# Kernel optimization log

Hardware: AMD Instinct MI355X
Metric: run time of the kernel (lower is better)

Reference implementation:

```python
import jax, jax.numpy as jnp
import numpy as np

N = 50000      # nodes
E = 600000     # edges
G = 256        # graphs in batch
H = 128        # hidden channels
EPS = 1e-5     # batchnorm eps


def gcn_conv(x, W, b, src, dst, n):
    """PyG GCNConv: h = x W; symmetric-normalized aggregation with self-loops."""
    h = x @ W  # [n, H]
    ones = jnp.ones(src.shape[0], dtype=x.dtype)
    deg = jax.ops.segment_sum(ones, dst, num_segments=n) + 1.0  # in-degree + self-loop
    dis = jax.lax.rsqrt(deg)  # deg^{-1/2}
    msg = (dis[src] * dis[dst])[:, None] * h[src]  # [E, H] gathered messages
    agg = jax.ops.segment_sum(msg, dst, num_segments=n)
    return agg + (dis * dis)[:, None] * h + b  # self-loop contribution + bias


def batch_norm(x, gamma, beta):
    m = x.mean(axis=0)
    v = x.var(axis=0)  # biased variance, as torch BN uses for normalization
    return gamma * (x - m) * jax.lax.rsqrt(v + EPS) + beta


def setup_inputs() -> dict:
    key = jax.random.key(0)
    ks = jax.random.split(key, 12)
    x = jax.random.normal(ks[0], (N, H), dtype=jnp.float32)
    edge_index = jax.random.randint(ks[1], (2, E), 0, N, dtype=jnp.int32)
    batch = jnp.sort(jax.random.randint(ks[2], (N,), 0, G, dtype=jnp.int32))
    s = 1.0 / np.sqrt(H)
    W1 = jax.random.uniform(ks[3], (H, H), jnp.float32, -s, s)
    b1 = jnp.zeros((H,), jnp.float32)
    g1 = jnp.ones((H,), jnp.float32)
    be1 = jnp.zeros((H,), jnp.float32)
    W2 = jax.random.uniform(ks[4], (H, H), jnp.float32, -s, s)
    b2 = jnp.zeros((H,), jnp.float32)
    g2 = jnp.ones((H,), jnp.float32)
    be2 = jnp.zeros((H,), jnp.float32)
    W3 = jax.random.uniform(ks[5], (H, H), jnp.float32, -s, s)
    b3 = jnp.zeros((H,), jnp.float32)
    Wl = jax.random.uniform(ks[6], (H, 1), jnp.float32, -s, s)
    bl = jnp.zeros((1,), jnp.float32)
    return {"x": x, "edge_index": edge_index, "batch": batch,
            "W1": W1, "b1": b1, "g1": g1, "be1": be1,
            "W2": W2, "b2": b2, "g2": g2, "be2": be2,
            "W3": W3, "b3": b3, "Wl": Wl, "bl": bl}


def reference(x, edge_index, batch, W1, b1, g1, be1, W2, b2, g2, be2, W3, b3, Wl, bl):
    src, dst = edge_index[0], edge_index[1]
    h = gcn_conv(x, W1, b1, src, dst, N)
    h = jax.nn.relu(batch_norm(h, g1, be1))  # dropout is identity in eval mode
    h = gcn_conv(h, W2, b2, src, dst, N)
    h = jax.nn.relu(batch_norm(h, g2, be2))
    h = jax.nn.relu(gcn_conv(h, W3, b3, src, dst, N))
    sums = jax.ops.segment_sum(h, batch, num_segments=G)           # [G, H]
    cnt = jax.ops.segment_sum(jnp.ones((N,), h.dtype), batch, num_segments=G)
    pooled = sums / jnp.maximum(cnt, 1.0)[:, None]                  # global mean pool
    return pooled @ Wl + bl                                         # [G, 1]
```

## Files before the change

kernel.cpp:

```cpp
#include <hip/hip_runtime.h>
#include <cstdint>

#define NN 50000
#define NE 600000
#define NGR 256
#define HD 128
#define HD2 64
#define BN_EPS 1e-5f

static __device__ __forceinline__ unsigned f2bf(float f) {
  unsigned u = __float_as_uint(f);
  return (u + 0x7FFFu + ((u >> 16) & 1u)) >> 16;
}
static __device__ __forceinline__ float bf_lo(unsigned v) {
  return __uint_as_float(v << 16);
}
static __device__ __forceinline__ float bf_hi(unsigned v) {
  return __uint_as_float(v & 0xFFFF0000u);
}

__global__ void k_zero(float4* __restrict__ p, int n4) {
  int i = blockIdx.x * blockDim.x + threadIdx.x;
  if (i < n4) p[i] = make_float4(0.f, 0.f, 0.f, 0.f);
}

__global__ void k_count(const int* __restrict__ dst, int* __restrict__ cnt) {
  int i = blockIdx.x * blockDim.x + threadIdx.x;
  if (i < NE) atomicAdd(&cnt[dst[i]], 1);
}

__global__ __launch_bounds__(1024) void k_scan1(const int* __restrict__ cnt,
                                                int* __restrict__ rowptr,
                                                int* __restrict__ aux,
                                                float* __restrict__ dis) {
  __shared__ int sd[1024];
  int tid = threadIdx.x;
  int i = blockIdx.x * 1024 + tid;
  int v = (i < NN) ? cnt[i] : 0;
  if (i < NN) dis[i] = 1.0f / sqrtf((float)v + 1.0f);
  sd[tid] = v;
  __syncthreads();
  for (int off = 1; off < 1024; off <<= 1) {
    int t = (tid >= off) ? sd[tid - off] : 0;
    __syncthreads();
    sd[tid] += t;
    __syncthreads();
  }
  if (i < NN) rowptr[i + 1] = sd[tid];
  if (tid == 1023) aux[blockIdx.x] = sd[1023];
}

__global__ void k_scan2(const int* __restrict__ aux, int* __restrict__ auxsc, int nchunks) {
  if (threadIdx.x == 0 && blockIdx.x == 0) {
    int run = 0;
    for (int c = 0; c < nchunks; ++c) { auxsc[c] = run; run += aux[c]; }
  }
}

__global__ void k_scan3(int* __restrict__ rowptr, const int* __restrict__ auxsc) {
  int i = blockIdx.x * blockDim.x + threadIdx.x;
  if (i < NN) rowptr[i + 1] += auxsc[i >> 10];
  if (i == 0) rowptr[0] = 0;
}

__global__ void k_fill(const int* __restrict__ src, const int* __restrict__ dst,
                       const int* __restrict__ rowptr, int* __restrict__ fillp,
                       int* __restrict__ colidx) {
  int i = blockIdx.x * blockDim.x + threadIdx.x;
  if (i < NE) {
    int d = dst[i];
    int p = rowptr[d] + atomicAdd(&fillp[d], 1);
    colidx[p] = src[i];
  }
}

template<bool BN>
__global__ __launch_bounds__(256) void k_gemm(
    const float* __restrict__ X, const float* __restrict__ W,
    const float* __restrict__ scale, const float* __restrict__ shift,
    const float* __restrict__ dis, unsigned* __restrict__ HS) {
  __shared__ float xt[64][36];
  __shared__ float wt[32][132];
  int tid = threadIdx.x;
  int tc = tid & 15;
  int tr = tid >> 4;
  int row0 = blockIdx.x * 64;
  int r0 = tr * 4;
  float acc[4][8];
#pragma unroll
  for (int i = 0; i < 4; ++i)
#pragma unroll
    for (int j = 0; j < 8; ++j) acc[i][j] = 0.f;

  int lr = tid >> 2;
  int lk = (tid & 3) * 8;
  int wk = tid >> 3;
  int wc = (tid & 7) * 16;

  for (int kk = 0; kk < HD; kk += 32) {
    float4 a0 = make_float4(0.f, 0.f, 0.f, 0.f);
    float4 a1 = make_float4(0.f, 0.f, 0.f, 0.f);
    int row = row0 + lr;
    if (row < NN) {
      const float* xp = &X[(size_t)row * HD + kk + lk];
      a0 = *(const float4*)xp;
      a1 = *(const float4*)(xp + 4);
    }
    if constexpr (BN) {
      float4 sc0 = *(const float4*)&scale[kk + lk];
      float4 sc1 = *(const float4*)&scale[kk + lk + 4];
      float4 sh0 = *(const float4*)&shift[kk + lk];
      float4 sh1 = *(const float4*)&shift[kk + lk + 4];
      a0.x = fmaxf(fmaf(sc0.x, a0.x, sh0.x), 0.f);
      a0.y = fmaxf(fmaf(sc0.y, a0.y, sh0.y), 0.f);
      a0.z = fmaxf(fmaf(sc0.z, a0.z, sh0.z), 0.f);
      a0.w = fmaxf(fmaf(sc0.w, a0.w, sh0.w), 0.f);
      a1.x = fmaxf(fmaf(sc1.x, a1.x, sh1.x), 0.f);
      a1.y = fmaxf(fmaf(sc1.y, a1.y, sh1.y), 0.f);
      a1.z = fmaxf(fmaf(sc1.z, a1.z, sh1.z), 0.f);
      a1.w = fmaxf(fmaf(sc1.w, a1.w, sh1.w), 0.f);
    }
    *(float4*)&xt[lr][lk] = a0;
    *(float4*)&xt[lr][lk + 4] = a1;
    const float* wp = &W[(size_t)(kk + wk) * HD + wc];
    *(float4*)&wt[wk][wc]      = *(const float4*)(wp);
    *(float4*)&wt[wk][wc + 4]  = *(const float4*)(wp + 4);
    *(float4*)&wt[wk][wc + 8]  = *(const float4*)(wp + 8);
    *(float4*)&wt[wk][wc + 12] = *(const float4*)(wp + 12);
    __syncthreads();
#pragma unroll 4
    for (int k = 0; k < 32; ++k) {
      float av[4];
#pragma unroll
      for (int i = 0; i < 4; ++i) av[i] = xt[r0 + i][k];
      float2 bv[4];
#pragma unroll
      for (int j = 0; j < 4; ++j) bv[j] = *(const float2*)&wt[k][tc * 2 + 32 * j];
#pragma unroll
      for (int i = 0; i < 4; ++i)
#pragma unroll
        for (int j = 0; j < 4; ++j) {
          acc[i][2 * j]     = fmaf(av[i], bv[j].x, acc[i][2 * j]);
          acc[i][2 * j + 1] = fmaf(av[i], bv[j].y, acc[i][2 * j + 1]);
        }
    }
    __syncthreads();
  }
#pragma unroll
  for (int i = 0; i < 4; ++i) {
    int row = row0 + r0 + i;
    if (row < NN) {
      float dv = dis[row];
#pragma unroll
      for (int j = 0; j < 4; ++j) {
        unsigned p = (f2bf(acc[i][2 * j + 1] * dv) << 16) | f2bf(acc[i][2 * j] * dv);
        HS[(size_t)row * HD2 + tc + 16 * j] = p;
      }
    }
  }
}

template<int MODE>
__global__ __launch_bounds__(256) void k_agg(
    const unsigned* __restrict__ HS, const float* __restrict__ dis,
    const int* __restrict__ rowptr, const int* __restrict__ colidx,
    const float* __restrict__ bias,
    float* __restrict__ AGG, float* __restrict__ stats,
    const int* __restrict__ batch, const float* __restrict__ Wl,
    float* __restrict__ gsum, float* __restrict__ gcnt) {
  __shared__ float red[4][128];
  int tid = threadIdx.x;
  int lane = tid & 63;
  int wv = tid >> 6;
  int c0 = lane * 2;
  float b0 = bias[c0], b1 = bias[c0 + 1];
  float wl0 = 0.f, wl1 = 0.f;
  if (MODE == 1) { wl0 = Wl[c0]; wl1 = Wl[c0 + 1]; }
  float ssum0 = 0.f, ssum1 = 0.f, ssq0 = 0.f, ssq1 = 0.f;
  int stride = gridDim.x * 4;
  for (int i = blockIdx.x * 4 + wv; i < NN; i += stride) {
    unsigned sv = HS[(size_t)i * HD2 + lane];
    float ax = bf_lo(sv), ay = bf_hi(sv);
    float bx = 0.f, by = 0.f;
    int e0 = rowptr[i], e1 = rowptr[i + 1];
    int e = e0;
    for (; e + 3 < e1; e += 4) {
      int s0 = colidx[e];
      int s1 = colidx[e + 1];
      int s2 = colidx[e + 2];
      int s3 = colidx[e + 3];
      unsigned h0 = HS[(size_t)s0 * HD2 + lane];
      unsigned h1 = HS[(size_t)s1 * HD2 + lane];
      unsigned h2 = HS[(size_t)s2 * HD2 + lane];
      unsigned h3 = HS[(size_t)s3 * HD2 + lane];
      ax += bf_lo(h0); ay += bf_hi(h0);
      bx += bf_lo(h1); by += bf_hi(h1);
      ax += bf_lo(h2); ay += bf_hi(h2);
      bx += bf_lo(h3); by += bf_hi(h3);
    }
    for (; e < e1; ++e) {
      int s0 = colidx[e];
      unsigned h0 = HS[(size_t)s0 * HD2 + lane];
      ax += bf_lo(h0); ay += bf_hi(h0);
    }
    float di = dis[i];
    float vx = fmaf(di, ax + bx, b0);
    float vy = fmaf(di, ay + by, b1);
    if (MODE == 0) {
      *(float2*)&AGG[(size_t)i * HD + c0] = make_float2(vx, vy);
      ssum0 += vx; ssum1 += vy;
      ssq0 = fmaf(vx, vx, ssq0);
      ssq1 = fmaf(vy, vy, ssq1);
    } else {
      vx = fmaxf(vx, 0.f);
      vy = fmaxf(vy, 0.f);
      float p = vx * wl0 + vy * wl1;
#pragma unroll
      for (int m = 32; m >= 1; m >>= 1) p += __shfl_xor(p, m);
      if (lane == 0) {
        int b = batch[i];
        atomicAdd(&gsum[b], p);
        atomicAdd(&gcnt[b], 1.0f);
      }
    }
  }
  if (MODE == 0) {
    red[wv][c0] = ssum0; red[wv][c0 + 1] = ssum1;
    __syncthreads();
    if (wv == 0) {
      float t0 = red[0][c0] + red[1][c0] + red[2][c0] + red[3][c0];
      float t1 = red[0][c0 + 1] + red[1][c0 + 1] + red[2][c0 + 1] + red[3][c0 + 1];
      atomicAdd(&stats[c0], t0);
      atomicAdd(&stats[c0 + 1], t1);
    }
    __syncthreads();
    red[wv][c0] = ssq0; red[wv][c0 + 1] = ssq1;
    __syncthreads();
    if (wv == 0) {
      float q0 = red[0][c0] + red[1][c0] + red[2][c0] + red[3][c0];
      float q1 = red[0][c0 + 1] + red[1][c0 + 1] + red[2][c0 + 1] + red[3][c0 + 1];
      atomicAdd(&stats[HD + c0], q0);
      atomicAdd(&stats[HD + c0 + 1], q1);
    }
  }
}

__global__ void k_bnfin(const float* __restrict__ stats, const float* __restrict__ gamma,
                        const float* __restrict__ beta, float* __restrict__ scale,
                        float* __restrict__ shift) {
  int c = threadIdx.x;
  float inv_n = 1.0f / (float)NN;
  float mean = stats[c] * inv_n;
  float var = stats[HD + c] * inv_n - mean * mean;
  float s = gamma[c] / sqrtf(var + BN_EPS);
  scale[c] = s;
  shift[c] = fmaf(-mean, s, beta[c]);
}

__global__ void k_final(const float* __restrict__ gsum, const float* __restrict__ gcnt,
                        const float* __restrict__ bl, float* __restrict__ out) {
  int g = threadIdx.x;
  out[g] = gsum[g] / fmaxf(gcnt[g], 1.0f) + bl[0];
}

extern "C" void kernel_launch(void* const* d_in, const int* in_sizes, int n_in,
                              void* d_out, int out_size, void* d_ws, size_t ws_size,
                              hipStream_t stream) {
  (void)in_sizes; (void)n_in; (void)out_size; (void)ws_size;
  const float* x   = (const float*)d_in[0];
  const int* ei    = (const int*)d_in[1];
  const int* batch = (const int*)d_in[2];
  const float* W1  = (const float*)d_in[3];
  const float* b1  = (const float*)d_in[4];
  const float* g1  = (const float*)d_in[5];
  const float* be1 = (const float*)d_in[6];
  const float* W2  = (const float*)d_in[7];
  const float* b2  = (const float*)d_in[8];
  const float* g2  = (const float*)d_in[9];
  const float* be2 = (const float*)d_in[10];
  const float* W3  = (const float*)d_in[11];
  const float* b3  = (const float*)d_in[12];
  const float* Wl  = (const float*)d_in[13];
  const float* bl  = (const float*)d_in[14];
  float* out = (float*)d_out;

  const int* srcv = ei;
  const int* dstv = ei + NE;

  unsigned* hs  = (unsigned*)d_ws;
  float* agg    = (float*)(hs + (size_t)NN * HD2);
  float* dis    = agg + (size_t)NN * HD;
  int*   rowptr = (int*)(dis + NN);
  int*   colidx = rowptr + (NN + 4);
  float* scale1 = (float*)(colidx + NE);
  float* shift1 = scale1 + HD;
  float* scale2 = shift1 + HD;
  float* shift2 = scale2 + HD;
  float* zbase  = shift2 + HD;
  int*   degc   = (int*)zbase;
  int*   fillp  = degc + NN;
  int*   aux    = fillp + NN;
  int*   auxsc  = aux + 64;
  float* stats1 = (float*)(auxsc + 64);
  float* stats2 = stats1 + 2 * HD;
  float* gsum   = stats2 + 2 * HD;
  float* gcnt   = gsum + NGR;
  float* zend   = gcnt + NGR;
  int n4 = (int)(((char*)zend - (char*)zbase) / 16);

  k_zero<<<(n4 + 255) / 256, 256, 0, stream>>>((float4*)zbase, n4);

  k_count<<<(NE + 255) / 256, 256, 0, stream>>>(dstv, degc);
  int nchunk = (NN + 1023) / 1024;
  k_scan1<<<nchunk, 1024, 0, stream>>>(degc, rowptr, aux, dis);
  k_scan2<<<1, 1, 0, stream>>>(aux, auxsc, nchunk);
  k_scan3<<<(NN + 255) / 256, 256, 0, stream>>>(rowptr, auxsc);
  k_fill<<<(NE + 255) / 256, 256, 0, stream>>>(srcv, dstv, rowptr, fillp, colidx);

  int gblk = (NN + 63) / 64;
  k_gemm<false><<<gblk, 256, 0, stream>>>(x, W1, nullptr, nullptr, dis, hs);
  k_agg<0><<<2048, 256, 0, stream>>>(hs, dis, rowptr, colidx, b1, agg, stats1,
                                     nullptr, nullptr, nullptr, nullptr);
  k_bnfin<<<1, HD, 0, stream>>>(stats1, g1, be1, scale1, shift1);
  k_gemm<true><<<gblk, 256, 0, stream>>>(agg, W2, scale1, shift1, dis, hs);
  k_agg<0><<<2048, 256, 0, stream>>>(hs, dis, rowptr, colidx, b2, agg, stats2,
                                     nullptr, nullptr, nullptr, nullptr);
  k_bnfin<<<1, HD, 0, stream>>>(stats2, g2, be2, scale2, shift2);
  k_gemm<true><<<gblk, 256, 0, stream>>>(agg, W3, scale2, shift2, dis, hs);
  k_agg<1><<<2048, 256, 0, stream>>>(hs, dis, rowptr, colidx, b3, nullptr, nullptr,
                                     batch, Wl, gsum, gcnt);
  k_final<<<1, NGR, 0, stream>>>(gsum, gcnt, bl, out);
}
```

Measured before the change: 732.0 us.

## Aggregate four nodes per wavefront with 16-byte gathers and atomic work queue

```diff
diff --git a/kernel.cpp b/kernel.cpp
--- a/kernel.cpp
+++ b/kernel.cpp
@@ -6,6 +6,7 @@
 #define NGR 256
 #define HD 128
 #define HD2 64
+#define NGRP 12500
 #define BN_EPS 1e-5f
 
 static __device__ __forceinline__ unsigned f2bf(float f) {
@@ -167,80 +168,109 @@
     const float* __restrict__ bias,
     float* __restrict__ AGG, float* __restrict__ stats,
     const int* __restrict__ batch, const float* __restrict__ Wl,
-    float* __restrict__ gsum, float* __restrict__ gcnt) {
-  __shared__ float red[4][128];
+    float* __restrict__ gsum, float* __restrict__ gcnt,
+    int* __restrict__ wq) {
+  __shared__ float red[16][128];
   int tid = threadIdx.x;
   int lane = tid & 63;
-  int wv = tid >> 6;
-  int c0 = lane * 2;
-  float b0 = bias[c0], b1 = bias[c0 + 1];
-  float wl0 = 0.f, wl1 = 0.f;
-  if (MODE == 1) { wl0 = Wl[c0]; wl1 = Wl[c0 + 1]; }
-  float ssum0 = 0.f, ssum1 = 0.f, ssq0 = 0.f, ssq1 = 0.f;
-  int stride = gridDim.x * 4;
-  for (int i = blockIdx.x * 4 + wv; i < NN; i += stride) {
-    unsigned sv = HS[(size_t)i * HD2 + lane];
-    float ax = bf_lo(sv), ay = bf_hi(sv);
-    float bx = 0.f, by = 0.f;
-    int e0 = rowptr[i], e1 = rowptr[i + 1];
-    int e = e0;
-    for (; e + 3 < e1; e += 4) {
-      int s0 = colidx[e];
-      int s1 = colidx[e + 1];
-      int s2 = colidx[e + 2];
-      int s3 = colidx[e + 3];
-      unsigned h0 = HS[(size_t)s0 * HD2 + lane];
-      unsigned h1 = HS[(size_t)s1 * HD2 + lane];
-      unsigned h2 = HS[(size_t)s2 * HD2 + lane];
-      unsigned h3 = HS[(size_t)s3 * HD2 + lane];
-      ax += bf_lo(h0); ay += bf_hi(h0);
-      bx += bf_lo(h1); by += bf_hi(h1);
-      ax += bf_lo(h2); ay += bf_hi(h2);
-      bx += bf_lo(h3); by += bf_hi(h3);
-    }
-    for (; e < e1; ++e) {
-      int s0 = colidx[e];
-      unsigned h0 = HS[(size_t)s0 * HD2 + lane];
-      ax += bf_lo(h0); ay += bf_hi(h0);
-    }
-    float di = dis[i];
-    float vx = fmaf(di, ax + bx, b0);
-    float vy = fmaf(di, ay + by, b1);
+  int il = lane & 15;
+  int q = lane >> 4;
+  int cbase = il * 8;
+  float ssum[8], ssq[8];
+#pragma unroll
+  for (int j = 0; j < 8; ++j) { ssum[j] = 0.f; ssq[j] = 0.f; }
+  float bia[8];
+  *(float4*)&bia[0] = *(const float4*)&bias[cbase];
+  *(float4*)&bia[4] = *(const float4*)&bias[cbase + 4];
+  float wl[8];
+  if (MODE == 1) {
+    *(float4*)&wl[0] = *(const float4*)&Wl[cbase];
+    *(float4*)&wl[4] = *(const float4*)&Wl[cbase + 4];
+  }
+  for (;;) {
+    int g = 0;
+    if (lane == 0) g = atomicAdd(wq, 1);
+    g = __builtin_amdgcn_readfirstlane(g);
+    if (g >= NGRP) break;
+    int n = g * 4 + q;
+    int e0 = rowptr[n], e1 = rowptr[n + 1];
+    int deg = e1 - e0;
+    int m = deg;
+    m = max(m, __shfl_xor(m, 16));
+    m = max(m, __shfl_xor(m, 32));
+    uint4 hs_ = *(const uint4*)&HS[(size_t)n * HD2 + il * 4];
+    float acc[8];
+    acc[0] = bf_lo(hs_.x); acc[1] = bf_hi(hs_.x);
+    acc[2] = bf_lo(hs_.y); acc[3] = bf_hi(hs_.y);
+    acc[4] = bf_lo(hs_.z); acc[5] = bf_hi(hs_.z);
+    acc[6] = bf_lo(hs_.w); acc[7] = bf_hi(hs_.w);
+    int ecl = max(e1 - 1, 0);
+    for (int k = 0; k < m; k += 2) {
+      int eA = e0 + k, eB = e0 + k + 1;
+      int iA = colidx[min(eA, ecl)];
+      int iB = colidx[min(eB, ecl)];
+      uint4 hA = *(const uint4*)&HS[(size_t)iA * HD2 + il * 4];
+      uint4 hB = *(const uint4*)&HS[(size_t)iB * HD2 + il * 4];
+      if (eA >= e1) { hA.x = 0u; hA.y = 0u; hA.z = 0u; hA.w = 0u; }
+      if (eB >= e1) { hB.x = 0u; hB.y = 0u; hB.z = 0u; hB.w = 0u; }
+      acc[0] += bf_lo(hA.x) + bf_lo(hB.x);
+      acc[1] += bf_hi(hA.x) + bf_hi(hB.x);
+      acc[2] += bf_lo(hA.y) + bf_lo(hB.y);
+      acc[3] += bf_hi(hA.y) + bf_hi(hB.y);
+      acc[4] += bf_lo(hA.z) + bf_lo(hB.z);
+      acc[5] += bf_hi(hA.z) + bf_hi(hB.z);
+      acc[6] += bf_lo(hA.w) + bf_lo(hB.w);
+      acc[7] += bf_hi(hA.w) + bf_hi(hB.w);
+    }
+    float di = dis[n];
     if (MODE == 0) {
-      *(float2*)&AGG[(size_t)i * HD + c0] = make_float2(vx, vy);
-      ssum0 += vx; ssum1 += vy;
-      ssq0 = fmaf(vx, vx, ssq0);
-      ssq1 = fmaf(vy, vy, ssq1);
+      float v[8];
+#pragma unroll
+      for (int j = 0; j < 8; ++j) {
+        v[j] = fmaf(di, acc[j], bia[j]);
+        ssum[j] += v[j];
+        ssq[j] = fmaf(v[j], v[j], ssq[j]);
+      }
+      *(float4*)&AGG[(size_t)n * HD + cbase]     = make_float4(v[0], v[1], v[2], v[3]);
+      *(float4*)&AGG[(size_t)n * HD + cbase + 4] = make_float4(v[4], v[5], v[6], v[7]);
     } else {
-      vx = fmaxf(vx, 0.f);
-      vy = fmaxf(vy, 0.f);
-      float p = vx * wl0 + vy * wl1;
-#pragma unroll
-      for (int m = 32; m >= 1; m >>= 1) p += __shfl_xor(p, m);
-      if (lane == 0) {
-        int b = batch[i];
+      float p = 0.f;
+#pragma unroll
+      for (int j = 0; j < 8; ++j) {
+        float v = fmaxf(fmaf(di, acc[j], bia[j]), 0.f);
+        p = fmaf(v, wl[j], p);
+      }
+      p += __shfl_xor(p, 8);
+      p += __shfl_xor(p, 4);
+      p += __shfl_xor(p, 2);
+      p += __shfl_xor(p, 1);
+      if (il == 0) {
+        int b = batch[n];
         atomicAdd(&gsum[b], p);
         atomicAdd(&gcnt[b], 1.0f);
       }
     }
   }
   if (MODE == 0) {
-    red[wv][c0] = ssum0; red[wv][c0 + 1] = ssum1;
-    __syncthreads();
-    if (wv == 0) {
-      float t0 = red[0][c0] + red[1][c0] + red[2][c0] + red[3][c0];
-      float t1 = red[0][c0 + 1] + red[1][c0 + 1] + red[2][c0 + 1] + red[3][c0 + 1];
-      atomicAdd(&stats[c0], t0);
-      atomicAdd(&stats[c0 + 1], t1);
-    }
-    __syncthreads();
-    red[wv][c0] = ssq0; red[wv][c0 + 1] = ssq1;
-    __syncthreads();
-    if (wv == 0) {
-      float q0 = red[0][c0] + red[1][c0] + red[2][c0] + red[3][c0];
-      float q1 = red[0][c0 + 1] + red[1][c0 + 1] + red[2][c0 + 1] + red[3][c0 + 1];
-      atomicAdd(&stats[HD + c0], q0);
-      atomicAdd(&stats[HD + c0 + 1], q1);
+    int r = (tid >> 6) * 4 + q;
+    *(float4*)&red[r][cbase]     = *(float4*)&ssum[0];
+    *(float4*)&red[r][cbase + 4] = *(float4*)&ssum[4];
+    __syncthreads();
+    if (tid < 128) {
+      float s = 0.f;
+#pragma unroll
+      for (int r2 = 0; r2 < 16; ++r2) s += red[r2][tid];
+      atomicAdd(&stats[tid], s);
+    }
+    __syncthreads();
+    *(float4*)&red[r][cbase]     = *(float4*)&ssq[0];
+    *(float4*)&red[r][cbase + 4] = *(float4*)&ssq[4];
+    __syncthreads();
+    if (tid < 128) {
+      float s = 0.f;
+#pragma unroll
+      for (int r2 = 0; r2 < 16; ++r2) s += red[r2][tid];
+      atomicAdd(&stats[HD + tid], s);
     }
   }
 }
@@ -301,7 +331,8 @@
   int*   fillp  = degc + NN;
   int*   aux    = fillp + NN;
   int*   auxsc  = aux + 64;
-  float* stats1 = (float*)(auxsc + 64);
+  int*   wq     = auxsc + 64;
+  float* stats1 = (float*)(wq + 4);
   float* stats2 = stats1 + 2 * HD;
   float* gsum   = stats2 + 2 * HD;
   float* gcnt   = gsum + NGR;
@@ -320,14 +351,14 @@
   int gblk = (NN + 63) / 64;
   k_gemm<false><<<gblk, 256, 0, stream>>>(x, W1, nullptr, nullptr, dis, hs);
   k_agg<0><<<2048, 256, 0, stream>>>(hs, dis, rowptr, colidx, b1, agg, stats1,
-                                     nullptr, nullptr, nullptr, nullptr);
+                                     nullptr, nullptr, nullptr, nullptr, wq);
   k_bnfin<<<1, HD, 0, stream>>>(stats1, g1, be1, scale1, shift1);
   k_gemm<true><<<gblk, 256, 0, stream>>>(agg, W2, scale1, shift1, dis, hs);
   k_agg<0><<<2048, 256, 0, stream>>>(hs, dis, rowptr, colidx, b2, agg, stats2,
-                                     nullptr, nullptr, nullptr, nullptr);
+                                     nullptr, nullptr, nullptr, nullptr, wq + 1);
   k_bnfin<<<1, HD, 0, stream>>>(stats2, g2, be2, scale2, shift2);
   k_gemm<true><<<gblk, 256, 0, stream>>>(agg, W3, scale2, shift2, dis, hs);
   k_agg<1><<<2048, 256, 0, stream>>>(hs, dis, rowptr, colidx, b3, nullptr, nullptr,
-                                     batch, Wl, gsum, gcnt);
+                                     batch, Wl, gsum, gcnt, wq + 2);
   k_final<<<1, NGR, 0, stream>>>(gsum, gcnt, bl, out);
 }
```

Result: slower. 1.073 ms (+46.6%).
